# Kernel tuning notes

Measured on AMD Instinct MI355X. Metric: run time of the kernel, lower is better.

The kernel has to match this reference:

```python
import jax, jax.numpy as jnp
import numpy as np

D_MODEL = 1024
NUM_HEADS = 16
HDIM = D_MODEL // NUM_HEADS
THETA = 10000.0


def setup_inputs() -> dict:
    key = jax.random.key(0)
    ks = jax.random.split(key, 5)
    bs, seq = 4, 2048
    std = np.sqrt(2.0 / (D_MODEL + D_MODEL))
    def w(k):
        # trunc_normal approximated by clipped normal (same distribution family)
        return jnp.clip(std * jax.random.normal(k, (D_MODEL, D_MODEL), jnp.float32), -3 * std, 3 * std)
    return {
        "x": jax.random.normal(ks[0], (bs, seq, D_MODEL), jnp.float32),
        "Wq": w(ks[1]), "Wk": w(ks[2]), "Wv": w(ks[3]), "Wo": w(ks[4]),
        "token_positions": jnp.arange(seq, dtype=jnp.int64),
    }


def _rope(x, token_positions):
    # x: (bs, H, S, hdim); rotate even/odd interleaved pairs
    inv_freq = THETA ** (-2.0 * jnp.arange(HDIM // 2, dtype=jnp.float32) / HDIM)
    freqs = token_positions.astype(jnp.float32)[:, None] * inv_freq[None, :]  # (S, hdim/2)
    cos, sin = jnp.cos(freqs), jnp.sin(freqs)
    x_even, x_odd = x[..., 0::2], x[..., 1::2]
    out_even = x_even * cos - x_odd * sin
    out_odd = x_odd * cos + x_even * sin
    # interleave back: stack on new last axis then reshape
    return jnp.stack([out_even, out_odd], axis=-1).reshape(x.shape)


def reference(x, Wq, Wk, Wv, Wo, token_positions):
    bs, seq, _ = x.shape
    q = (x @ Wq.T).reshape(bs, seq, NUM_HEADS, HDIM).transpose(0, 2, 1, 3)
    k = (x @ Wk.T).reshape(bs, seq, NUM_HEADS, HDIM).transpose(0, 2, 1, 3)
    v = (x @ Wv.T).reshape(bs, seq, NUM_HEADS, HDIM).transpose(0, 2, 1, 3)
    q = _rope(q, token_positions)
    k = _rope(k, token_positions)
    scores = jnp.einsum("bhsd,bhtd->bhst", q, k) / jnp.sqrt(jnp.float32(HDIM))
    mask = jnp.tril(jnp.ones((seq, seq), dtype=bool))
    scores = jnp.where(mask, scores, -jnp.inf)
    attn = jax.nn.softmax(scores, axis=-1)
    out = jnp.einsum("bhst,bhtd->bhsd", attn, v)
    out = out.transpose(0, 2, 1, 3).reshape(bs, seq, D_MODEL)
    return out @ Wo.T
```

## Files before the change

### kernel.cpp

```cpp
#include <hip/hip_runtime.h>
#include <hip/hip_fp16.h>

typedef _Float16 half8 __attribute__((ext_vector_type(8)));
typedef _Float16 half4 __attribute__((ext_vector_type(4)));
typedef _Float16 half2v __attribute__((ext_vector_type(2)));
typedef float f32x4 __attribute__((ext_vector_type(4)));
typedef float f32x8v __attribute__((ext_vector_type(8)));
typedef float f32x16 __attribute__((ext_vector_type(16)));

#define SEQ   2048
#define DM    1024
#define NH    16
#define HD    64
#define BSZ   4

#if __has_builtin(__builtin_amdgcn_exp2f)
#define EXP2(x) __builtin_amdgcn_exp2f(x)
#else
#define EXP2(x) exp2f(x)
#endif

#define QSCALE 0.1803368801f
#define ROPE_C 0.41524101186f

__device__ __forceinline__ void gload16(const void* g, void* l) {
  __builtin_amdgcn_global_load_lds((const __attribute__((address_space(1))) void*)g,
                                   (__attribute__((address_space(3))) void*)l,
                                   16, 0, 0);
}

__global__ void cvt4(const float* __restrict__ src, _Float16* __restrict__ dst, int n4) {
  int i = blockIdx.x * blockDim.x + threadIdx.x;
  if (i < n4) {
    float4 v = ((const float4*)src)[i];
    half4 o = { (_Float16)v.x, (_Float16)v.y, (_Float16)v.z, (_Float16)v.w };
    ((half4*)dst)[i] = o;
  }
}

template<int MODE>
__global__ __launch_bounds__(256)
void gemm_hk(const _Float16* __restrict__ A, const _Float16* __restrict__ B,
             _Float16* __restrict__ oQ, _Float16* __restrict__ oK,
             _Float16* __restrict__ oVt, float* __restrict__ oF,
             const int* __restrict__ tp) {
  __shared__ _Float16 As[2][128*32];
  __shared__ _Float16 Bs[2][128*32];
  const int tid  = threadIdx.x;
  const int wid  = tid >> 6, lane = tid & 63;
  const int wm   = wid >> 1, wn = wid & 1;
  const int fr   = lane & 15, fg = lane >> 4;
  const long m0  = (long)blockIdx.x * 128;
  const long n0  = (long)blockIdx.y * 128;
  const int lrow = lane >> 2;
  const int lcol = (lane & 3) * 8;
  const _Float16* ga0 = A + (m0 + wid*32 + lrow) * 1024 + lcol;
  const _Float16* gb0 = B + (n0 + wid*32 + lrow) * 1024 + lcol;
  const int lofs = wid*32*32;

  f32x4 acc[4][4] = {};

  gload16(ga0,           &As[0][lofs]);
  gload16(ga0 + 16*1024, &As[0][lofs + 16*32]);
  gload16(gb0,           &Bs[0][lofs]);
  gload16(gb0 + 16*1024, &Bs[0][lofs + 16*32]);
  __syncthreads();

  int cur = 0;
  for (int k0 = 0; k0 < 1024; k0 += 32) {
    if (k0 + 32 < 1024) {
      gload16(ga0 + k0 + 32,           &As[cur^1][lofs]);
      gload16(ga0 + k0 + 32 + 16*1024, &As[cur^1][lofs + 16*32]);
      gload16(gb0 + k0 + 32,           &Bs[cur^1][lofs]);
      gload16(gb0 + k0 + 32 + 16*1024, &Bs[cur^1][lofs + 16*32]);
    }
    half8 af[4], bf[4];
#pragma unroll
    for (int i = 0; i < 4; ++i) {
      af[i] = *(const half8*)&As[cur][(wm*64 + i*16 + fr)*32 + fg*8];
      bf[i] = *(const half8*)&Bs[cur][(wn*64 + i*16 + fr)*32 + fg*8];
    }
    __builtin_amdgcn_s_setprio(1);
#pragma unroll
    for (int i = 0; i < 4; ++i)
#pragma unroll
      for (int j = 0; j < 4; ++j)
        acc[i][j] = __builtin_amdgcn_mfma_f32_16x16x32_f16(af[i], bf[j], acc[i][j], 0, 0, 0);
    __builtin_amdgcn_s_setprio(0);
    __syncthreads();
    cur ^= 1;
  }

  if (MODE == 0) {
    const int which = (int)(n0 >> 10);
    const int nloc0 = ((int)n0 & 1023) + wn*64;
    const bool odd = fr & 1;
#pragma unroll
    for (int i = 0; i < 4; ++i) {
      const long r0 = m0 + wm*64 + i*16 + fg*4;
      const int  bb = (int)(r0 >> 11);
      const int  s  = (int)(r0 & 2047);
#pragma unroll
      for (int j = 0; j < 4; ++j) {
        const int nl = nloc0 + j*16 + fr;
        const int h  = nl >> 6, d = nl & 63;
        const long bh = (long)(bb*NH + h);
        if (which == 2) {
          half4 pk = { (_Float16)acc[i][j][0], (_Float16)acc[i][j][1],
                       (_Float16)acc[i][j][2], (_Float16)acc[i][j][3] };
          *(half4*)&oVt[(bh*HD + d)*SEQ + s] = pk;
        } else {
          const float inv = exp2f(-ROPE_C * (float)(d >> 1));
#pragma unroll
          for (int r = 0; r < 4; ++r) {
            const float v = acc[i][j][r];
            const float p = __shfl_xor(v, 1);
            float sn, cs;
            __sincosf((float)tp[s + r] * inv, &sn, &cs);
            const float out = odd ? (v*cs + p*sn) : (v*cs - p*sn);
            if (which == 0)
              oQ[(bh*SEQ + s + r)*HD + d] = (_Float16)(out * QSCALE);
            else
              oK[(bh*SEQ + s + r)*HD + d] = (_Float16)out;
          }
        }
      }
    }
  } else {
#pragma unroll
    for (int i = 0; i < 4; ++i) {
      const long r0 = m0 + wm*64 + i*16 + fg*4;
#pragma unroll
      for (int j = 0; j < 4; ++j) {
        const long col = n0 + wn*64 + j*16 + fr;
#pragma unroll
        for (int r = 0; r < 4; ++r)
          oF[(r0 + r)*DM + col] = acc[i][j][r];
      }
    }
  }
}

__global__ __launch_bounds__(256, 2)
void fattn(const _Float16* __restrict__ Q, const _Float16* __restrict__ K,
           const _Float16* __restrict__ Vt, _Float16* __restrict__ O) {
  __shared__ _Float16 Ks[2][64*64];
  __shared__ _Float16 Vs[2][64*64];
  __shared__ _Float16 Ps[4][32*64];
  const int tid = threadIdx.x, wid = tid >> 6, lane = tid & 63;
  const int q31 = lane & 31, hi = lane >> 5;
  const int bh = blockIdx.x, b = bh >> 4, h = bh & 15;
  const int y = blockIdx.y;
  const int qs_[2] = { (15 - y)*128 + wid*32, y*128 + wid*32 };
  const _Float16* Qb = Q + (long)bh * SEQ * HD;
  const _Float16* Kb = K + (long)bh * SEQ * HD;
  const _Float16* Vb = Vt + (long)bh * HD * SEQ;

  half8 qf[2][4];
#pragma unroll
  for (int s = 0; s < 2; ++s)
#pragma unroll
    for (int c = 0; c < 4; ++c)
      qf[s][c] = *(const half8*)&Qb[(qs_[s] + q31)*HD + c*16 + hi*8];

  f32x16 oacc[2][2] = {};
  float m_s[2] = { -1e30f, -1e30f }, l_s[2] = { 0.f, 0.f };

  const int srow = lane >> 3;
  const int sc16 = (lane & 7) ^ srow;
  const int r1 = wid*16 + srow, r2 = r1 + 8;

  char* Pb = (char*)&Ps[wid][0];
  const int swp = (q31 & 7) << 4;
  const int nt = (15 - y)*2 + 2;

  gload16(Kb + (long)r1*HD + sc16*8, &Ks[0][(wid*16)*64]);
  gload16(Kb + (long)r2*HD + sc16*8, &Ks[0][(wid*16 + 8)*64]);
  gload16(Vb + (long)r1*SEQ + sc16*8, &Vs[0][(wid*16)*64]);
  gload16(Vb + (long)r2*SEQ + sc16*8, &Vs[0][(wid*16 + 8)*64]);
  __syncthreads();

  int cur = 0;
  for (int t = 0; t < nt; ++t) {
    const int kv0 = t * 64;

    if (t + 1 < nt) {
      const int nkv = kv0 + 64;
      gload16(Kb + (long)(nkv + r1)*HD + sc16*8, &Ks[cur^1][(wid*16)*64]);
      gload16(Kb + (long)(nkv + r2)*HD + sc16*8, &Ks[cur^1][(wid*16 + 8)*64]);
      gload16(Vb + (long)r1*SEQ + nkv + sc16*8,  &Vs[cur^1][(wid*16)*64]);
      gload16(Vb + (long)r2*SEQ + nkv + sc16*8,  &Vs[cur^1][(wid*16 + 8)*64]);
    }

    const char* Kc = (const char*)&Ks[cur][0];
    const char* Vc = (const char*)&Vs[cur][0];

#pragma unroll
    for (int hh = 0; hh < 2; ++hh) {
      const int kvb = kv0 + 32*hh;
#pragma unroll
      for (int s = 0; s < 2; ++s) {
        const int qs0 = qs_[s];
        if (kvb > qs0 + 31) continue;

        f32x16 sa = {};
        __builtin_amdgcn_s_setprio(1);
#pragma unroll
        for (int c = 0; c < 4; ++c) {
          const int row = 32*hh + q31;
          const half8 kf = *(const half8*)(Kc + row*128 + ((c*32 + hi*16) ^ ((row & 7) << 4)));
          sa = __builtin_amdgcn_mfma_f32_32x32x16_f16(kf, qf[s][c], sa, 0, 0, 0);
        }
        __builtin_amdgcn_s_setprio(0);

        if (kvb + 31 > qs0) {
          const int thr = qs0 + q31 - kvb - 4*hi;
#pragma unroll
          for (int r = 0; r < 16; ++r) {
            const int cr = (r & 3) + 8*(r >> 2);
            if (cr > thr) sa[r] = -1e30f;
          }
        }

        f32x8v mx8;
#pragma unroll
        for (int i = 0; i < 8; ++i) mx8[i] = fmaxf(sa[i], sa[i+8]);
        f32x4 mx4;
#pragma unroll
        for (int i = 0; i < 4; ++i) mx4[i] = fmaxf(mx8[i], mx8[i+4]);
        float pm = fmaxf(fmaxf(mx4[0], mx4[1]), fmaxf(mx4[2], mx4[3]));
        pm = fmaxf(pm, __shfl_xor(pm, 32));

        if (!__all(pm <= m_s[s] + 8.0f)) {
          const float mn = fmaxf(m_s[s], pm);
          const float fac = EXP2(m_s[s] - mn);
          m_s[s] = mn;
          l_s[s] *= fac;
          oacc[s][0] *= fac;
          oacc[s][1] *= fac;
        }
        const float mrow = m_s[s];

#pragma unroll
        for (int r = 0; r < 16; ++r) sa[r] = EXP2(sa[r] - mrow);

        f32x8v s8;
#pragma unroll
        for (int i = 0; i < 8; ++i) s8[i] = sa[i] + sa[i+8];
        f32x4 s4v;
#pragma unroll
        for (int i = 0; i < 4; ++i) s4v[i] = s8[i] + s8[i+4];
        float ps = (s4v[0] + s4v[1]) + (s4v[2] + s4v[3]);
        ps += __shfl_xor(ps, 32);
        l_s[s] += ps;

#pragma unroll
        for (int g = 0; g < 4; ++g) {
          half2v lo  = (half2v)__builtin_amdgcn_cvt_pkrtz(sa[4*g+0], sa[4*g+1]);
          half2v hi2 = (half2v)__builtin_amdgcn_cvt_pkrtz(sa[4*g+2], sa[4*g+3]);
          half4 p4 = __builtin_shufflevector(lo, hi2, 0, 1, 2, 3);
          *(half4*)(Pb + q31*128 + ((g*16 + hi*8) ^ swp)) = p4;
        }

        __builtin_amdgcn_s_setprio(1);
#pragma unroll
        for (int ks = 0; ks < 2; ++ks) {
          const half8 pf = *(const half8*)(Pb + q31*128 + ((ks*32 + hi*16) ^ swp));
#pragma unroll
          for (int nd = 0; nd < 2; ++nd) {
            const int row = nd*32 + q31;
            const half8 vf = *(const half8*)(Vc + row*128 +
                              ((hh*64 + ks*32 + hi*16) ^ ((row & 7) << 4)));
            oacc[s][nd] = __builtin_amdgcn_mfma_f32_32x32x16_f16(vf, pf, oacc[s][nd], 0, 0, 0);
          }
        }
        __builtin_amdgcn_s_setprio(0);
      }
    }

    __syncthreads();
    cur ^= 1;
  }

#pragma unroll
  for (int s = 0; s < 2; ++s) {
    const float rl = __builtin_amdgcn_rcpf(l_s[s]);
    _Float16* orow = O + ((long)b*SEQ + (qs_[s] + q31))*DM + h*64;
#pragma unroll
    for (int nd = 0; nd < 2; ++nd)
#pragma unroll
      for (int g = 0; g < 4; ++g) {
        half2v lo  = (half2v)__builtin_amdgcn_cvt_pkrtz(oacc[s][nd][4*g+0]*rl, oacc[s][nd][4*g+1]*rl);
        half2v hi2 = (half2v)__builtin_amdgcn_cvt_pkrtz(oacc[s][nd][4*g+2]*rl, oacc[s][nd][4*g+3]*rl);
        half4 o4 = __builtin_shufflevector(lo, hi2, 0, 1, 2, 3);
        *(half4*)&orow[nd*32 + g*8 + 4*hi] = o4;
      }
  }
}

extern "C" void kernel_launch(void* const* d_in, const int* in_sizes, int n_in,
                              void* d_out, int out_size, void* d_ws, size_t ws_size,
                              hipStream_t stream) {
  const float* x  = (const float*)d_in[0];
  const float* Wq = (const float*)d_in[1];
  const float* Wk = (const float*)d_in[2];
  const float* Wv = (const float*)d_in[3];
  const float* Wo = (const float*)d_in[4];
  const int*   tp = (const int*)d_in[5];
  float* out = (float*)d_out;

  char* ws = (char*)d_ws;
  _Float16* xh   = (_Float16*)(ws);
  _Float16* Wqkv = (_Float16*)(ws + (16u << 20));
  _Float16* Woh  = (_Float16*)(ws + (22u << 20));
  _Float16* Qb   = (_Float16*)(ws + (24u << 20));
  _Float16* Kb   = (_Float16*)(ws + (40u << 20));
  _Float16* Vtb  = (_Float16*)(ws + (56u << 20));
  _Float16* attn = (_Float16*)(ws + (72u << 20));

  cvt4<<<8192, 256, 0, stream>>>(x,  xh, 2097152);
  cvt4<<<1024, 256, 0, stream>>>(Wq, Wqkv,               262144);
  cvt4<<<1024, 256, 0, stream>>>(Wk, Wqkv + (1u << 20),  262144);
  cvt4<<<1024, 256, 0, stream>>>(Wv, Wqkv + (2u << 20),  262144);
  cvt4<<<1024, 256, 0, stream>>>(Wo, Woh,                262144);

  gemm_hk<0><<<dim3(64, 24), 256, 0, stream>>>(xh, Wqkv, Qb, Kb, Vtb, nullptr, tp);
  fattn<<<dim3(64, 8), 256, 0, stream>>>(Qb, Kb, Vtb, attn);
  gemm_hk<1><<<dim3(64, 8), 256, 0, stream>>>(attn, Woh, nullptr, nullptr, nullptr, out, nullptr);
}
```

Baseline: 182.0 us.

## Keep softmax P in registers via permuted K rows; merge weight conversions

The attention kernel permutes which K rows feed the QK^T MFMA so the score accumulator layout lines up with the B-operand layout of the PV MFMA. This lets P be packed straight into half8 registers instead of going through a shared-memory round trip, and the causal-mask index math is updated to match. Separately, the four weight fp32-to-fp16 conversion launches are merged into one 2D-grid launch to cut launch overhead. The permutation has to be exactly right for correctness, and it changes the LDS read pattern for K.

```diff
diff --git a/kernel.cpp b/kernel.cpp
--- a/kernel.cpp
+++ b/kernel.cpp
@@ -36,6 +36,18 @@
     half4 o = { (_Float16)v.x, (_Float16)v.y, (_Float16)v.z, (_Float16)v.w };
     ((half4*)dst)[i] = o;
   }
+}
+
+__global__ void cvtW(const float* __restrict__ s0, const float* __restrict__ s1,
+                     const float* __restrict__ s2, const float* __restrict__ s3,
+                     _Float16* __restrict__ dqkv, _Float16* __restrict__ dO) {
+  const int y = blockIdx.y;
+  const float* src = (y == 0) ? s0 : (y == 1) ? s1 : (y == 2) ? s2 : s3;
+  _Float16* dst = (y < 3) ? (dqkv + (long)y * (1u << 20)) : dO;
+  int i = blockIdx.x * blockDim.x + threadIdx.x;
+  float4 v = ((const float4*)src)[i];
+  half4 o = { (_Float16)v.x, (_Float16)v.y, (_Float16)v.z, (_Float16)v.w };
+  ((half4*)dst)[i] = o;
 }
 
 template<int MODE>
@@ -146,9 +158,9 @@
            const _Float16* __restrict__ Vt, _Float16* __restrict__ O) {
   __shared__ _Float16 Ks[2][64*64];
   __shared__ _Float16 Vs[2][64*64];
-  __shared__ _Float16 Ps[4][32*64];
   const int tid = threadIdx.x, wid = tid >> 6, lane = tid & 63;
   const int q31 = lane & 31, hi = lane >> 5;
+  const int qp  = (q31 & 19) | ((q31 & 4) << 1) | ((q31 & 8) >> 1);
   const int bh = blockIdx.x, b = bh >> 4, h = bh & 15;
   const int y = blockIdx.y;
   const int qs_[2] = { (15 - y)*128 + wid*32, y*128 + wid*32 };
@@ -170,8 +182,6 @@
   const int sc16 = (lane & 7) ^ srow;
   const int r1 = wid*16 + srow, r2 = r1 + 8;
 
-  char* Pb = (char*)&Ps[wid][0];
-  const int swp = (q31 & 7) << 4;
   const int nt = (15 - y)*2 + 2;
 
   gload16(Kb + (long)r1*HD + sc16*8, &Ks[0][(wid*16)*64]);
@@ -207,17 +217,17 @@
         __builtin_amdgcn_s_setprio(1);
 #pragma unroll
         for (int c = 0; c < 4; ++c) {
-          const int row = 32*hh + q31;
+          const int row = 32*hh + qp;
           const half8 kf = *(const half8*)(Kc + row*128 + ((c*32 + hi*16) ^ ((row & 7) << 4)));
           sa = __builtin_amdgcn_mfma_f32_32x32x16_f16(kf, qf[s][c], sa, 0, 0, 0);
         }
         __builtin_amdgcn_s_setprio(0);
 
         if (kvb + 31 > qs0) {
-          const int thr = qs0 + q31 - kvb - 4*hi;
+          const int thr = qs0 + q31 - kvb - 8*hi;
 #pragma unroll
           for (int r = 0; r < 16; ++r) {
-            const int cr = (r & 3) + 8*(r >> 2);
+            const int cr = (r & 3) + 4*((r >> 2) & 1) + 16*(r >> 3);
             if (cr > thr) sa[r] = -1e30f;
           }
         }
@@ -254,18 +264,19 @@
         ps += __shfl_xor(ps, 32);
         l_s[s] += ps;
 
+        half8 pf0, pf1;
 #pragma unroll
         for (int g = 0; g < 4; ++g) {
-          half2v lo  = (half2v)__builtin_amdgcn_cvt_pkrtz(sa[4*g+0], sa[4*g+1]);
-          half2v hi2 = (half2v)__builtin_amdgcn_cvt_pkrtz(sa[4*g+2], sa[4*g+3]);
-          half4 p4 = __builtin_shufflevector(lo, hi2, 0, 1, 2, 3);
-          *(half4*)(Pb + q31*128 + ((g*16 + hi*8) ^ swp)) = p4;
+          half2v t0 = (half2v)__builtin_amdgcn_cvt_pkrtz(sa[2*g],   sa[2*g+1]);
+          half2v t1 = (half2v)__builtin_amdgcn_cvt_pkrtz(sa[8+2*g], sa[8+2*g+1]);
+          pf0[2*g]   = t0[0];  pf0[2*g+1] = t0[1];
+          pf1[2*g]   = t1[0];  pf1[2*g+1] = t1[1];
         }
 
         __builtin_amdgcn_s_setprio(1);
 #pragma unroll
         for (int ks = 0; ks < 2; ++ks) {
-          const half8 pf = *(const half8*)(Pb + q31*128 + ((ks*32 + hi*16) ^ swp));
+          const half8 pf = ks ? pf1 : pf0;
 #pragma unroll
           for (int nd = 0; nd < 2; ++nd) {
             const int row = nd*32 + q31;
@@ -318,11 +329,8 @@
   _Float16* Vtb  = (_Float16*)(ws + (56u << 20));
   _Float16* attn = (_Float16*)(ws + (72u << 20));
 
-  cvt4<<<8192, 256, 0, stream>>>(x,  xh, 2097152);
-  cvt4<<<1024, 256, 0, stream>>>(Wq, Wqkv,               262144);
-  cvt4<<<1024, 256, 0, stream>>>(Wk, Wqkv + (1u << 20),  262144);
-  cvt4<<<1024, 256, 0, stream>>>(Wv, Wqkv + (2u << 20),  262144);
-  cvt4<<<1024, 256, 0, stream>>>(Wo, Woh,                262144);
+  cvt4<<<8192, 256, 0, stream>>>(x, xh, 2097152);
+  cvtW<<<dim3(1024, 4), 256, 0, stream>>>(Wq, Wk, Wv, Wo, Wqkv, Woh);
 
   gemm_hk<0><<<dim3(64, 24), 256, 0, stream>>>(xh, Wqkv, Qb, Kb, Vtb, nullptr, tp);
   fattn<<<dim3(64, 8), 256, 0, stream>>>(Qb, Kb, Vtb, attn);
```

New measurement: 170.9 us. 1.07x faster.
